# Kernel tuning notes

Hardware: AMD Instinct MI355X
Metric: run time of the kernel (lower is better)

The kernel has to match this reference:

```python
import jax, jax.numpy as jnp
import numpy as np

B, L = 128, 256          # trees per batch, leaves per tree (perfect binary tree)
V, D, H = 50000, 300, 512  # vocab, word_dim, tree_input_dim == output_dim


def setup_inputs() -> dict:
    key = jax.random.key(0)
    ks = jax.random.split(key, 6)
    token_ids = jax.random.randint(ks[0], (B, L), 0, V)
    scale_e = np.sqrt(3.0 / D).astype(np.float32)  # reset_embedding uniform(-scale, scale)
    emb_table = jax.random.uniform(ks[1], (V, D), jnp.float32, -scale_e, scale_e)
    s = 0.02
    Wx = jax.random.normal(ks[2], (D, 5 * H), jnp.float32) * s  # leaf input -> (i, fl, fr, o, u)
    Ul = jax.random.normal(ks[3], (H, 5 * H), jnp.float32) * s  # left child h
    Ur = jax.random.normal(ks[4], (H, 5 * H), jnp.float32) * s  # right child h
    b = jax.random.normal(ks[5], (5 * H,), jnp.float32) * s
    return {"token_ids": token_ids, "emb_table": emb_table, "Wx": Wx, "Ul": Ul, "Ur": Ur, "b": b}


def _cell(xproj, hl, hr, cl, cr, Ul, Ur, b):
    # Binary tree-LSTM cell (Tai et al., fold-style) with per-child forget gates.
    g = xproj + hl @ Ul + hr @ Ur + b            # [..., 5H]
    i, fl, fr, o, u = jnp.split(g, 5, axis=-1)
    c = jax.nn.sigmoid(i) * jnp.tanh(u) + jax.nn.sigmoid(fl) * cl + jax.nn.sigmoid(fr) * cr
    h = jax.nn.sigmoid(o) * jnp.tanh(c)
    return h, c


def reference(token_ids, emb_table, Wx, Ul, Ur, b):
    # Eval mode: all dropouts are identity.
    x = emb_table[token_ids]                      # [B, L, D] leaf word embeddings
    z = jnp.zeros((B, L, H), x.dtype)             # leaf children states are zero
    h, c = _cell(x @ Wx, z, z, z, z, Ul, Ur, b)   # all leaves at once
    hs = [h]
    # Level-wise bottom-up over the perfect binary tree (internal nodes: inputs=None).
    while h.shape[1] > 1:
        hl, hr = h[:, 0::2], h[:, 1::2]
        cl, cr = c[:, 0::2], c[:, 1::2]
        h, c = _cell(jnp.float32(0.0), hl, hr, cl, cr, Ul, Ur, b)
        hs.append(h)
    # Collected hidden states of all 2L-1 nodes (leaves first, then levels up to root).
    return jnp.concatenate(hs, axis=1)            # [B, 2L-1, H]
```

## Files before the change

kernel.cpp:

```cpp
#include <hip/hip_runtime.h>
#include <hip/hip_bf16.h>
#include <cstdint>

#define BB 128
#define LL 256
#define DD 300
#define HH 512
#define TOUT 511
#define NGATE 2560

typedef __attribute__((ext_vector_type(8))) short bf16x8;
typedef __attribute__((ext_vector_type(4))) float f32x4;

__device__ __forceinline__ float rcpf(float x){ return __builtin_amdgcn_rcpf(x); }
__device__ __forceinline__ float ex2f(float x){ return __builtin_amdgcn_exp2f(x); }
__device__ __forceinline__ float sigf(float x){ return rcpf(1.0f + ex2f(x * -1.44269504f)); }
__device__ __forceinline__ float tanh_fast(float x){ return 1.0f - 2.0f*rcpf(ex2f(x * 2.88539008f) + 1.0f); }

__device__ __forceinline__ void load_lds16(const void* g, void* l) {
  __builtin_amdgcn_global_load_lds(
      (const __attribute__((address_space(1))) unsigned int*)g,
      (__attribute__((address_space(3))) unsigned int*)l, 16, 0, 0);
}

#define VMWAIT(n) asm volatile("s_waitcnt vmcnt(" #n ")" ::: "memory")
#define LGKM0()   asm volatile("s_waitcnt lgkmcnt(0)" ::: "memory")

__global__ __launch_bounds__(256) void prep_weights(
    const float* __restrict__ Wx, const float* __restrict__ Ul, const float* __restrict__ Ur,
    __hip_bfloat16* __restrict__ Wb0t, __hip_bfloat16* __restrict__ Wb1t)
{
  const int z = blockIdx.z;
  const float* src; __hip_bfloat16* dst; int Ksrc, Kdst, koff;
  if (z == 0) { if (blockIdx.x >= 5) return; src = Wx; dst = Wb0t; Ksrc = DD; Kdst = 320; koff = 0; }
  else if (z == 1) { src = Ul; dst = Wb1t; Ksrc = HH; Kdst = 1024; koff = 0; }
  else { src = Ur; dst = Wb1t; Ksrc = HH; Kdst = 1024; koff = 512; }

  __shared__ float t[64][65];
  const int tid = threadIdx.x;
  const int k0 = blockIdx.x * 64;
  const int n0 = blockIdx.y * 64;
  #pragma unroll
  for (int p = 0; p < 16; ++p) {
    int lin = p*256 + tid;
    int ki = lin >> 6, nj = lin & 63;
    t[ki][nj] = (k0 + ki < Ksrc) ? src[(size_t)(k0+ki)*NGATE + n0 + nj] : 0.f;
  }
  __syncthreads();
  #pragma unroll
  for (int p = 0; p < 16; ++p) {
    int lin = p*256 + tid;
    int ni = lin >> 6, kj = lin & 63;
    dst[(size_t)(n0+ni)*Kdst + koff + k0 + kj] = __float2bfloat16(t[kj][ni]);
  }
}

__global__ void embed_cvt(const int* __restrict__ tok, const float* __restrict__ emb,
                          __hip_bfloat16* __restrict__ A0)
{
  int k = blockIdx.x * 64 + threadIdx.x;
  int r = blockIdx.y * 4 + threadIdx.y;
  int tk = tok[r];
  float v = (k < DD) ? emb[(size_t)tk*DD + k] : 0.f;
  A0[(size_t)r*320 + k] = __float2bfloat16(v);
}

__global__ __launch_bounds__(512, 2) void gemm_l0(
    const __hip_bfloat16* __restrict__ A, const __hip_bfloat16* __restrict__ Wt,
    const float* __restrict__ bias,
    float* __restrict__ out, __hip_bfloat16* __restrict__ hout, float* __restrict__ cout)
{
  constexpr int P  = 4;
  constexpr int NT = 10;
  constexpr int HBYT = 36864;
  constexpr size_t rowK = 640;
  constexpr size_t panStride = 256 * rowK;
  __shared__ __align__(16) char lds[4*HBYT];

  const int tid  = threadIdx.x;
  const int lane = tid & 63;
  const int wid  = tid >> 6;
  const int wm   = wid >> 2;
  const int wn   = wid & 3;
  const int bid  = blockIdx.x;
  const int m    = (bid & 7) + ((bid >> 6) << 3);
  const int s    = (bid >> 3) & 7;
  const int n0   = s * 64;

  const bool isAwave = (wid < 4);
  const char* gsrc[5];
  int ldst0;
  if (isAwave) {
    #pragma unroll
    for (int i = 0; i < 4; ++i) {
      int gi  = wid*4 + i;
      int row = gi*16 + (lane >> 2);
      int cs  = (lane & 3) ^ ((row >> 1) & 3);
      gsrc[i] = (const char*)A + (size_t)m*P*panStride + (size_t)row*rowK + cs*16;
    }
    gsrc[4] = nullptr;
    ldst0 = (wid*4)*1024 + lane*16;
  } else {
    #pragma unroll
    for (int i = 0; i < 5; ++i) {
      int bj   = (wid-4)*5 + i;
      int rowb = bj*16 + (lane >> 2);
      int cs   = (lane & 3) ^ ((rowb >> 1) & 3);
      int grow = (rowb >> 6)*512 + n0 + (rowb & 63);
      gsrc[i] = (const char*)Wt + (size_t)grow*rowK + cs*16;
    }
    ldst0 = 16384 + ((wid-4)*5)*1024 + lane*16;
  }

  f32x4 acc[8][5];
  #pragma unroll
  for (int mf = 0; mf < 8; ++mf)
    #pragma unroll
    for (int g5 = 0; g5 < 5; ++g5)
      acc[mf][g5] = (f32x4){0.f,0.f,0.f,0.f};

  int ts = 0, Tstage = 0;
  auto stage = [&](){
    char* base = lds + (size_t)(Tstage & 3)*HBYT + ldst0;
    const size_t kb = (size_t)ts*64;
    if (isAwave) {
      #pragma unroll
      for (int i = 0; i < 4; ++i) load_lds16(gsrc[i] + kb, base + i*1024);
    } else {
      #pragma unroll
      for (int i = 0; i < 5; ++i) load_lds16(gsrc[i] + kb, base + i*1024);
    }
    ++Tstage;
    if (++ts == NT) {
      ts = 0;
      if (isAwave) {
        #pragma unroll
        for (int i = 0; i < 4; ++i) gsrc[i] += panStride;
      }
    }
  };

  stage(); stage(); stage();

  const int jg = n0 + wn*16 + (lane & 15);
  float bia[5];
  #pragma unroll
  for (int g5 = 0; g5 < 5; ++g5) bia[g5] = bias[g5*HH + jg];

  constexpr int total = P * NT;
  #pragma unroll 1
  for (int p = 0; p < P; ++p) {
    #pragma unroll 1
    for (int t = 0; t < NT; ++t) {
      const int Tc = p*NT + t;
      if (Tc + 3 <= total)      { if (isAwave) VMWAIT(8); else VMWAIT(10); }
      else if (Tc + 2 <= total) { if (isAwave) VMWAIT(4); else VMWAIT(5); }
      else                      { VMWAIT(0); }
      LGKM0();
      __builtin_amdgcn_s_barrier();

      const char* Ab = lds + (size_t)(Tc & 3)*HBYT;
      const char* Bb = Ab + 16384;
      const int q = lane >> 4;

      bf16x8 b[5];
      #pragma unroll
      for (int g5 = 0; g5 < 5; ++g5) {
        int c = g5*64 + wn*16 + (lane & 15);
        b[g5] = *(const bf16x8*)(Bb + c*64 + ((q ^ ((c >> 1) & 3))*16));
      }
      bf16x8 a[4];
      #pragma unroll
      for (int i = 0; i < 4; ++i) {
        int r = wm*128 + i*16 + (lane & 15);
        a[i] = *(const bf16x8*)(Ab + r*64 + ((q ^ ((r >> 1) & 3))*16));
      }
      if (Tstage < total) stage();
      __builtin_amdgcn_sched_barrier(0);
      __builtin_amdgcn_s_setprio(1);
      #pragma unroll
      for (int mf = 0; mf < 4; ++mf)
        #pragma unroll
        for (int g5 = 0; g5 < 5; ++g5)
          acc[mf][g5] = __builtin_amdgcn_mfma_f32_16x16x32_bf16(a[mf], b[g5], acc[mf][g5], 0, 0, 0);
      __builtin_amdgcn_s_setprio(0);

      #pragma unroll
      for (int i = 0; i < 4; ++i) {
        int r = wm*128 + (4+i)*16 + (lane & 15);
        a[i] = *(const bf16x8*)(Ab + r*64 + ((q ^ ((r >> 1) & 3))*16));
      }
      __builtin_amdgcn_sched_barrier(0);
      __builtin_amdgcn_s_setprio(1);
      #pragma unroll
      for (int mf = 0; mf < 4; ++mf)
        #pragma unroll
        for (int g5 = 0; g5 < 5; ++g5)
          acc[4+mf][g5] = __builtin_amdgcn_mfma_f32_16x16x32_bf16(a[mf], b[g5], acc[4+mf][g5], 0, 0, 0);
      __builtin_amdgcn_s_setprio(0);
    }

    const int r0 = (m*P + p) * 256;
    #pragma unroll
    for (int mf = 0; mf < 8; ++mf) {
      #pragma unroll
      for (int v = 0; v < 4; ++v) {
        int rr = r0 + wm*128 + mf*16 + (lane >> 4)*4 + v;
        float gi  = acc[mf][0][v] + bia[0];
        float go  = acc[mf][3][v] + bia[3];
        float gu  = acc[mf][4][v] + bia[4];
        float cc = sigf(gi)*tanh_fast(gu);
        float hh = sigf(go)*tanh_fast(cc);
        int b = rr >> 8;
        int t2 = rr & 255;
        out[((size_t)b*TOUT + t2)*HH + jg] = hh;
        hout[(size_t)rr*HH + jg] = __float2bfloat16(hh);
        cout[(size_t)rr*HH + jg] = cc;
        acc[mf][0][v]=0.f; acc[mf][1][v]=0.f; acc[mf][2][v]=0.f;
        acc[mf][3][v]=0.f; acc[mf][4][v]=0.f;
      }
    }
  }
}

__global__ __launch_bounds__(512, 2) void gemm_big(
    const __hip_bfloat16* __restrict__ A, const __hip_bfloat16* __restrict__ Wt,
    int K, const float* __restrict__ bias, const float* __restrict__ cprev,
    float* __restrict__ out, __hip_bfloat16* __restrict__ hout, float* __restrict__ cout,
    int lkshift, int sc)
{
  constexpr int HBYT = 36864;
  __shared__ __align__(16) char lds[4*HBYT];

  const int tid  = threadIdx.x;
  const int lane = tid & 63;
  const int wid  = tid >> 6;
  const int wm   = wid >> 2;
  const int wn   = wid & 3;
  const int bid  = blockIdx.x;
  const int m    = (bid & 7) + ((bid >> 6) << 3);
  const int s    = (bid >> 3) & 7;
  const int r0   = m * 256;
  const int n0   = s * 64;
  const size_t rowK = (size_t)K * 2;

  const int gi0 = (wid < 4) ? wid*5 : 20 + (wid-4)*4;
  const char* gsrc[5];
  #pragma unroll
  for (int i = 0; i < 5; ++i) {
    int gi = gi0 + i;
    if (gi < 16) {
      int row = gi*16 + (lane >> 2);
      int cs  = (lane & 3) ^ ((row >> 1) & 3);
      gsrc[i] = (const char*)A + (size_t)(r0 + row)*rowK + cs*16;
    } else {
      int rowb = (gi-16)*16 + (lane >> 2);
      int cs   = (lane & 3) ^ ((rowb >> 1) & 3);
      int grow = (rowb >> 6)*512 + n0 + (rowb & 63);
      gsrc[i] = (const char*)Wt + (size_t)grow*rowK + cs*16;
    }
  }
  const int ldst0 = gi0*1024 + lane*16;

  f32x4 acc[8][5];
  #pragma unroll
  for (int mf = 0; mf < 8; ++mf)
    #pragma unroll
    for (int g5 = 0; g5 < 5; ++g5)
      acc[mf][g5] = (f32x4){0.f,0.f,0.f,0.f};

  const int nt = K >> 5;
  auto stage = [&](int t){
    char* base = lds + (size_t)(t & 3)*HBYT + ldst0;
    const size_t kb = (size_t)t*64;
    if (wid < 4) {
      #pragma unroll
      for (int i = 0; i < 5; ++i) load_lds16(gsrc[i] + kb, base + i*1024);
    } else {
      #pragma unroll
      for (int i = 0; i < 4; ++i) load_lds16(gsrc[i] + kb, base + i*1024);
    }
  };

  stage(0); stage(1); stage(2);

  for (int t = 0; t < nt; ++t) {
    if (t + 2 < nt)      { if (wid < 4) VMWAIT(10); else VMWAIT(8); }
    else if (t + 1 < nt) { if (wid < 4) VMWAIT(5);  else VMWAIT(4); }
    else                 { VMWAIT(0); }
    LGKM0();
    __builtin_amdgcn_s_barrier();

    const char* Ab = lds + (size_t)(t & 3)*HBYT;
    const char* Bb = Ab + 16384;
    const int q = lane >> 4;

    bf16x8 b[5];
    #pragma unroll
    for (int g5 = 0; g5 < 5; ++g5) {
      int c = g5*64 + wn*16 + (lane & 15);
      b[g5] = *(const bf16x8*)(Bb + c*64 + ((q ^ ((c >> 1) & 3))*16));
    }
    bf16x8 a[4];
    #pragma unroll
    for (int i = 0; i < 4; ++i) {
      int r = wm*128 + i*16 + (lane & 15);
      a[i] = *(const bf16x8*)(Ab + r*64 + ((q ^ ((r >> 1) & 3))*16));
    }
    if (t + 3 < nt) stage(t + 3);
    __builtin_amdgcn_sched_barrier(0);
    __builtin_amdgcn_s_setprio(1);
    #pragma unroll
    for (int mf = 0; mf < 4; ++mf)
      #pragma unroll
      for (int g5 = 0; g5 < 5; ++g5)
        acc[mf][g5] = __builtin_amdgcn_mfma_f32_16x16x32_bf16(a[mf], b[g5], acc[mf][g5], 0, 0, 0);
    __builtin_amdgcn_s_setprio(0);

    #pragma unroll
    for (int i = 0; i < 4; ++i) {
      int r = wm*128 + (4+i)*16 + (lane & 15);
      a[i] = *(const bf16x8*)(Ab + r*64 + ((q ^ ((r >> 1) & 3))*16));
    }
    __builtin_amdgcn_sched_barrier(0);
    __builtin_amdgcn_s_setprio(1);
    #pragma unroll
    for (int mf = 0; mf < 4; ++mf)
      #pragma unroll
      for (int g5 = 0; g5 < 5; ++g5)
        acc[4+mf][g5] = __builtin_amdgcn_mfma_f32_16x16x32_bf16(a[mf], b[g5], acc[4+mf][g5], 0, 0, 0);
    __builtin_amdgcn_s_setprio(0);
  }

  const int Lmask = (1 << lkshift) - 1;
  const int jg = n0 + wn*16 + (lane & 15);
  float bia[5];
  #pragma unroll
  for (int g5 = 0; g5 < 5; ++g5) bia[g5] = bias[g5*HH + jg];
  #pragma unroll
  for (int mf = 0; mf < 8; ++mf) {
    #pragma unroll
    for (int v = 0; v < 4; ++v) {
      int rr = r0 + wm*128 + mf*16 + (lane >> 4)*4 + v;
      float gi  = acc[mf][0][v] + bia[0];
      float gfl = acc[mf][1][v] + bia[1];
      float gfr = acc[mf][2][v] + bia[2];
      float go  = acc[mf][3][v] + bia[3];
      float gu  = acc[mf][4][v] + bia[4];
      float cl = 0.f, cr = 0.f;
      if (cprev) {
        cl = cprev[(size_t)(2*rr)*HH + jg];
        cr = cprev[(size_t)(2*rr)*HH + HH + jg];
      }
      float cc = sigf(gi)*tanh_fast(gu) + sigf(gfl)*cl + sigf(gfr)*cr;
      float hh = sigf(go)*tanh_fast(cc);
      int b = rr >> lkshift;
      int t = rr & Lmask;
      out[((size_t)b*TOUT + sc + t)*HH + jg] = hh;
      hout[(size_t)rr*HH + jg] = __float2bfloat16(hh);
      cout[(size_t)rr*HH + jg] = cc;
    }
  }
}

__global__ __launch_bounds__(512, 2) void gemm_tail(
    const __hip_bfloat16* __restrict__ A, const __hip_bfloat16* __restrict__ Wt,
    const float* __restrict__ bias, const float* __restrict__ cprev,
    float* __restrict__ out, __hip_bfloat16* __restrict__ hout, float* __restrict__ cout,
    int lkshift, int sc, int numM)
{
  constexpr int ABYTES = 16384;
  constexpr int BUFS   = ABYTES + 40960;
  __shared__ __align__(16) char lds[2*BUFS];

  const int tid  = threadIdx.x;
  const int lane = tid & 63;
  const int wid  = tid >> 6;
  const int wm   = wid >> 2;
  const int wn   = wid & 3;
  const int bid  = blockIdx.x;
  int m, s;
  if (numM >= 8) { m = (bid & 7) + ((bid >> 6) << 3); s = (bid >> 3) & 7; }
  else           { m = bid % numM;  s = bid / numM; }
  const int r0   = m * 128;
  const int n0   = s * 64;
  constexpr size_t rowK = 2048;

  const int srow = lane >> 3;
  const int gq   = (lane & 7) ^ srow;
  const char* gsrc[7];
  #pragma unroll
  for (int ii = 0; ii < 7; ++ii) {
    int issue = wid*7 + ii;
    if (issue < 16) {
      int r = issue*8 + srow;
      gsrc[ii] = (const char*)A + (size_t)(r0 + r)*rowK + (size_t)gq*16;
    } else {
      int c = (issue-16)*8 + srow;
      int grow = (c >> 6)*512 + n0 + (c & 63);
      gsrc[ii] = (const char*)Wt + (size_t)grow*rowK + (size_t)gq*16;
    }
  }
  const int ldst0 = (wid*7)*1024 + lane*16;

  f32x4 acc[4][5];
  #pragma unroll
  for (int mf = 0; mf < 4; ++mf)
    #pragma unroll
    for (int g5 = 0; g5 < 5; ++g5)
      acc[mf][g5] = (f32x4){0.f,0.f,0.f,0.f};

  auto stage = [&](int buf, int kt){
    char* base = lds + buf*BUFS + ldst0;
    const size_t kb = (size_t)kt*128;
    #pragma unroll
    for (int ii = 0; ii < 7; ++ii) load_lds16(gsrc[ii] + kb, base + ii*1024);
  };

  stage(0, 0);
  int cur = 0;
  for (int kt = 0; kt < 16; ++kt) {
    if (kt + 1 < 16) {
      stage(cur ^ 1, kt + 1);
      VMWAIT(7);
    } else {
      VMWAIT(0);
    }
    __builtin_amdgcn_s_barrier();

    const char* Ab = lds + cur*BUFS;
    const char* Bb = Ab + ABYTES;
    #pragma unroll
    for (int s2 = 0; s2 < 2; ++s2) {
      const int qb = s2*4 + (lane >> 4);
      bf16x8 b[5];
      #pragma unroll
      for (int g5 = 0; g5 < 5; ++g5) {
        int c = g5*64 + wn*16 + (lane & 15);
        b[g5] = *(const bf16x8*)(Bb + c*128 + ((qb ^ (c & 7))*16));
      }
      __builtin_amdgcn_s_setprio(1);
      #pragma unroll
      for (int mf = 0; mf < 4; ++mf) {
        int r = wm*64 + mf*16 + (lane & 15);
        bf16x8 av = *(const bf16x8*)(Ab + r*128 + ((qb ^ (r & 7))*16));
        #pragma unroll
        for (int g5 = 0; g5 < 5; ++g5)
          acc[mf][g5] = __builtin_amdgcn_mfma_f32_16x16x32_bf16(av, b[g5], acc[mf][g5], 0, 0, 0);
      }
      __builtin_amdgcn_s_setprio(0);
    }
    __builtin_amdgcn_s_barrier();
    cur ^= 1;
  }

  const int Lmask = (1 << lkshift) - 1;
  const int jg = n0 + wn*16 + (lane & 15);
  float bia[5];
  #pragma unroll
  for (int g5 = 0; g5 < 5; ++g5) bia[g5] = bias[g5*HH + jg];
  #pragma unroll
  for (int mf = 0; mf < 4; ++mf) {
    #pragma unroll
    for (int v = 0; v < 4; ++v) {
      int rr = r0 + wm*64 + mf*16 + (lane >> 4)*4 + v;
      float gi  = acc[mf][0][v] + bia[0];
      float gfl = acc[mf][1][v] + bia[1];
      float gfr = acc[mf][2][v] + bia[2];
      float go  = acc[mf][3][v] + bia[3];
      float gu  = acc[mf][4][v] + bia[4];
      float cl = cprev[(size_t)(2*rr)*HH + jg];
      float cr = cprev[(size_t)(2*rr)*HH + HH + jg];
      float cc = sigf(gi)*tanh_fast(gu) + sigf(gfl)*cl + sigf(gfr)*cr;
      float hh = sigf(go)*tanh_fast(cc);
      int b = rr >> lkshift;
      int t = rr & Lmask;
      out[((size_t)b*TOUT + sc + t)*HH + jg] = hh;
      hout[(size_t)rr*HH + jg] = __float2bfloat16(hh);
      cout[(size_t)rr*HH + jg] = cc;
    }
  }
}

extern "C" void kernel_launch(void* const* d_in, const int* in_sizes, int n_in,
                              void* d_out, int out_size, void* d_ws, size_t ws_size,
                              hipStream_t stream) {
  (void)in_sizes; (void)n_in; (void)out_size; (void)ws_size;
  const int*   tok  = (const int*)d_in[0];
  const float* emb  = (const float*)d_in[1];
  const float* Wx   = (const float*)d_in[2];
  const float* Ul   = (const float*)d_in[3];
  const float* Ur   = (const float*)d_in[4];
  const float* bias = (const float*)d_in[5];
  float* out = (float*)d_out;

  char* ws = (char*)d_ws;
  size_t off = 0;
  __hip_bfloat16* Wb0t = (__hip_bfloat16*)(ws + off); off += (size_t)NGATE*320*2;
  __hip_bfloat16* Wb1t = (__hip_bfloat16*)(ws + off); off += (size_t)NGATE*1024*2;
  __hip_bfloat16* hA   = (__hip_bfloat16*)(ws + off); off += (size_t)32768*HH*2;
  __hip_bfloat16* hB   = (__hip_bfloat16*)(ws + off); off += (size_t)16384*HH*2;
  float*          cA   = (float*)(ws + off);          off += (size_t)32768*HH*4;
  float*          cB   = (float*)(ws + off);          off += (size_t)16384*HH*4;
  __hip_bfloat16* A0   = (__hip_bfloat16*)cB;

  prep_weights<<<dim3(8, 40, 3), 256, 0, stream>>>(Wx, Ul, Ur, Wb0t, Wb1t);
  embed_cvt<<<dim3(5, 8192), dim3(64,4), 0, stream>>>(tok, emb, A0);

  gemm_l0<<<256, 512, 0, stream>>>(A0, Wb0t, bias, out, hA, cA);
  gemm_big<<<(16384/256)*8, 512, 0, stream>>>(hA, Wb1t, 1024, bias, cA,
                                              out, hB, cB, 7, 256);
  gemm_big<<<(8192/256)*8, 512, 0, stream>>>(hB, Wb1t, 1024, bias, cB,
                                             out, hA, cA, 6, 384);
  for (int k = 3; k <= 8; ++k) {
    int M = 32768 >> k;
    int sc = HH - (HH >> k);
    const __hip_bfloat16* Ain = (k & 1) ? hA : hB;
    __hip_bfloat16*       hO  = (k & 1) ? hB : hA;
    const float*          cI  = (k & 1) ? cA : cB;
    float*                cO  = (k & 1) ? cB : cA;
    int numM = M / 128;
    gemm_tail<<<numM*8, 512, 0, stream>>>(Ain, Wb1t, bias, cI,
                                          out, hO, cO, 8 - k, sc, numM);
  }
}
```

Before: 411.2 us.

## Add specialized level-1 GEMM kernel and vectorize embedding gather

Replaces the generic gemm_big launch for tree level 1 with a dedicated gemm_l1 kernel. It treats each pair of sibling rows as one 1024-wide K row (rowK 2048 bytes), processes two 256-row panels per block, and keeps the four-stage LDS pipeline used by gemm_l0. The embedding gather now has each thread load eight floats with float4 reads and store eight bf16 values in one vector write, instead of one element per thread. The specialized kernel adds code duplication and changes the grid to 256 blocks, which may alter occupancy and load balance.

Result: no change. 411.3 us (+0.0%).

```diff
diff --git a/kernel.cpp b/kernel.cpp
--- a/kernel.cpp
+++ b/kernel.cpp
@@ -55,14 +55,30 @@
   }
 }
 
-__global__ void embed_cvt(const int* __restrict__ tok, const float* __restrict__ emb,
-                          __hip_bfloat16* __restrict__ A0)
+__global__ __launch_bounds__(256) void embed_cvt(
+    const int* __restrict__ tok, const float* __restrict__ emb,
+    __hip_bfloat16* __restrict__ A0)
 {
-  int k = blockIdx.x * 64 + threadIdx.x;
-  int r = blockIdx.y * 4 + threadIdx.y;
+  int idx = blockIdx.x*256 + threadIdx.x;
+  int r  = idx / 40;
+  int ck = (idx - r*40) * 8;
   int tk = tok[r];
-  float v = (k < DD) ? emb[(size_t)tk*DD + k] : 0.f;
-  A0[(size_t)r*320 + k] = __float2bfloat16(v);
+  const float* erow = emb + (size_t)tk*DD;
+  float v[8];
+  if (ck + 8 <= DD) {
+    float4 lo = *reinterpret_cast<const float4*>(erow + ck);
+    float4 hi = *reinterpret_cast<const float4*>(erow + ck + 4);
+    v[0]=lo.x; v[1]=lo.y; v[2]=lo.z; v[3]=lo.w;
+    v[4]=hi.x; v[5]=hi.y; v[6]=hi.z; v[7]=hi.w;
+  } else {
+    #pragma unroll
+    for (int j = 0; j < 8; ++j) { int k = ck + j; v[j] = (k < DD) ? erow[k] : 0.f; }
+  }
+  bf16x8 o;
+  #pragma unroll
+  for (int j = 0; j < 8; ++j)
+    o[j] = (short)__bfloat16_as_ushort(__float2bfloat16(v[j]));
+  *reinterpret_cast<bf16x8*>(&A0[(size_t)r*320 + ck]) = o;
 }
 
 __global__ __launch_bounds__(512, 2) void gemm_l0(
@@ -214,6 +230,168 @@
         int b = rr >> 8;
         int t2 = rr & 255;
         out[((size_t)b*TOUT + t2)*HH + jg] = hh;
+        hout[(size_t)rr*HH + jg] = __float2bfloat16(hh);
+        cout[(size_t)rr*HH + jg] = cc;
+        acc[mf][0][v]=0.f; acc[mf][1][v]=0.f; acc[mf][2][v]=0.f;
+        acc[mf][3][v]=0.f; acc[mf][4][v]=0.f;
+      }
+    }
+  }
+}
+
+__global__ __launch_bounds__(512, 2) void gemm_l1(
+    const __hip_bfloat16* __restrict__ A, const __hip_bfloat16* __restrict__ Wt,
+    const float* __restrict__ bias, const float* __restrict__ cprev,
+    float* __restrict__ out, __hip_bfloat16* __restrict__ hout, float* __restrict__ cout)
+{
+  constexpr int P  = 2;
+  constexpr int NT = 32;
+  constexpr int HBYT = 36864;
+  constexpr size_t rowK = 2048;
+  constexpr size_t panStride = 256 * rowK;
+  __shared__ __align__(16) char lds[4*HBYT];
+
+  const int tid  = threadIdx.x;
+  const int lane = tid & 63;
+  const int wid  = tid >> 6;
+  const int wm   = wid >> 2;
+  const int wn   = wid & 3;
+  const int bid  = blockIdx.x;
+  const int m    = (bid & 7) + ((bid >> 6) << 3);
+  const int s    = (bid >> 3) & 7;
+  const int n0   = s * 64;
+
+  const bool isAwave = (wid < 4);
+  const char* gsrc[5];
+  int ldst0;
+  if (isAwave) {
+    #pragma unroll
+    for (int i = 0; i < 4; ++i) {
+      int gi  = wid*4 + i;
+      int row = gi*16 + (lane >> 2);
+      int cs  = (lane & 3) ^ ((row >> 1) & 3);
+      gsrc[i] = (const char*)A + (size_t)m*P*panStride + (size_t)row*rowK + cs*16;
+    }
+    gsrc[4] = nullptr;
+    ldst0 = (wid*4)*1024 + lane*16;
+  } else {
+    #pragma unroll
+    for (int i = 0; i < 5; ++i) {
+      int bj   = (wid-4)*5 + i;
+      int rowb = bj*16 + (lane >> 2);
+      int cs   = (lane & 3) ^ ((rowb >> 1) & 3);
+      int grow = (rowb >> 6)*512 + n0 + (rowb & 63);
+      gsrc[i] = (const char*)Wt + (size_t)grow*rowK + cs*16;
+    }
+    ldst0 = 16384 + ((wid-4)*5)*1024 + lane*16;
+  }
+
+  f32x4 acc[8][5];
+  #pragma unroll
+  for (int mf = 0; mf < 8; ++mf)
+    #pragma unroll
+    for (int g5 = 0; g5 < 5; ++g5)
+      acc[mf][g5] = (f32x4){0.f,0.f,0.f,0.f};
+
+  int ts = 0, Tstage = 0;
+  auto stage = [&](){
+    char* base = lds + (size_t)(Tstage & 3)*HBYT + ldst0;
+    const size_t kb = (size_t)ts*64;
+    if (isAwave) {
+      #pragma unroll
+      for (int i = 0; i < 4; ++i) load_lds16(gsrc[i] + kb, base + i*1024);
+    } else {
+      #pragma unroll
+      for (int i = 0; i < 5; ++i) load_lds16(gsrc[i] + kb, base + i*1024);
+    }
+    ++Tstage;
+    if (++ts == NT) {
+      ts = 0;
+      if (isAwave) {
+        #pragma unroll
+        for (int i = 0; i < 4; ++i) gsrc[i] += panStride;
+      }
+    }
+  };
+
+  stage(); stage(); stage();
+
+  const int jg = n0 + wn*16 + (lane & 15);
+  float bia[5];
+  #pragma unroll
+  for (int g5 = 0; g5 < 5; ++g5) bia[g5] = bias[g5*HH + jg];
+
+  constexpr int total = P * NT;
+  #pragma unroll 1
+  for (int p = 0; p < P; ++p) {
+    #pragma unroll 1
+    for (int t = 0; t < NT; ++t) {
+      const int Tc = p*NT + t;
+      if (Tc + 3 <= total)      { if (isAwave) VMWAIT(8); else VMWAIT(10); }
+      else if (Tc + 2 <= total) { if (isAwave) VMWAIT(4); else VMWAIT(5); }
+      else                      { VMWAIT(0); }
+      LGKM0();
+      __builtin_amdgcn_s_barrier();
+
+      const char* Ab = lds + (size_t)(Tc & 3)*HBYT;
+      const char* Bb = Ab + 16384;
+      const int q = lane >> 4;
+
+      bf16x8 b[5];
+      #pragma unroll
+      for (int g5 = 0; g5 < 5; ++g5) {
+        int c = g5*64 + wn*16 + (lane & 15);
+        b[g5] = *(const bf16x8*)(Bb + c*64 + ((q ^ ((c >> 1) & 3))*16));
+      }
+      bf16x8 a[4];
+      #pragma unroll
+      for (int i = 0; i < 4; ++i) {
+        int r = wm*128 + i*16 + (lane & 15);
+        a[i] = *(const bf16x8*)(Ab + r*64 + ((q ^ ((r >> 1) & 3))*16));
+      }
+      if (Tstage < total) stage();
+      __builtin_amdgcn_sched_barrier(0);
+      __builtin_amdgcn_s_setprio(1);
+      #pragma unroll
+      for (int mf = 0; mf < 4; ++mf)
+        #pragma unroll
+        for (int g5 = 0; g5 < 5; ++g5)
+          acc[mf][g5] = __builtin_amdgcn_mfma_f32_16x16x32_bf16(a[mf], b[g5], acc[mf][g5], 0, 0, 0);
+      __builtin_amdgcn_s_setprio(0);
+
+      #pragma unroll
+      for (int i = 0; i < 4; ++i) {
+        int r = wm*128 + (4+i)*16 + (lane & 15);
+        a[i] = *(const bf16x8*)(Ab + r*64 + ((q ^ ((r >> 1) & 3))*16));
+      }
+      __builtin_amdgcn_sched_barrier(0);
+      __builtin_amdgcn_s_setprio(1);
+      #pragma unroll
+      for (int mf = 0; mf < 4; ++mf)
+        #pragma unroll
+        for (int g5 = 0; g5 < 5; ++g5)
+          acc[4+mf][g5] = __builtin_amdgcn_mfma_f32_16x16x32_bf16(a[mf], b[g5], acc[4+mf][g5], 0, 0, 0);
+      __builtin_amdgcn_s_setprio(0);
+    }
+
+    const int r0 = (m*P + p) * 256;
+    #pragma unroll
+    for (int mf = 0; mf < 8; ++mf) {
+      #pragma unroll
+      for (int v = 0; v < 4; ++v) {
+        int rr = r0 + wm*128 + mf*16 + (lane >> 4)*4 + v;
+        float gi  = acc[mf][0][v] + bia[0];
+        float gfl = acc[mf][1][v] + bia[1];
+        float gfr = acc[mf][2][v] + bia[2];
+        float go  = acc[mf][3][v] + bia[3];
+        float gu  = acc[mf][4][v] + bia[4];
+        float cl = cprev[(size_t)(2*rr)*HH + jg];
+        float cr = cprev[(size_t)(2*rr)*HH + HH + jg];
+        float cc = sigf(gi)*tanh_fast(gu) + sigf(gfl)*cl + sigf(gfr)*cr;
+        float hh = sigf(go)*tanh_fast(cc);
+        int b = rr >> 7;
+        int t2 = rr & 127;
+        out[((size_t)b*TOUT + 256 + t2)*HH + jg] = hh;
         hout[(size_t)rr*HH + jg] = __float2bfloat16(hh);
         cout[(size_t)rr*HH + jg] = cc;
         acc[mf][0][v]=0.f; acc[mf][1][v]=0.f; acc[mf][2][v]=0.f;
@@ -505,11 +683,10 @@
   __hip_bfloat16* A0   = (__hip_bfloat16*)cB;
 
   prep_weights<<<dim3(8, 40, 3), 256, 0, stream>>>(Wx, Ul, Ur, Wb0t, Wb1t);
-  embed_cvt<<<dim3(5, 8192), dim3(64,4), 0, stream>>>(tok, emb, A0);
+  embed_cvt<<<(32768*40)/256, 256, 0, stream>>>(tok, emb, A0);
 
   gemm_l0<<<256, 512, 0, stream>>>(A0, Wb0t, bias, out, hA, cA);
-  gemm_big<<<(16384/256)*8, 512, 0, stream>>>(hA, Wb1t, 1024, bias, cA,
-                                              out, hB, cB, 7, 256);
+  gemm_l1<<<256, 512, 0, stream>>>(hA, Wb1t, bias, cA, out, hB, cB);
   gemm_big<<<(8192/256)*8, 512, 0, stream>>>(hB, Wb1t, 1024, bias, cB,
                                              out, hA, cA, 6, 384);
   for (int k = 3; k <= 8; ++k) {
```
